# Performance work log

Measured on AMD Instinct MI355X. Metric: run time of the kernel, lower is better.

The kernel has to match this reference:

```python
import jax, jax.numpy as jnp
import numpy as np

EPS = 1e-5
N_NODES = 100000


def setup_inputs() -> dict:
    key = jax.random.key(0)
    ks = jax.random.split(key, 24)
    N, F = N_NODES, 64
    E = 1600000
    inp = {
        "x": jax.random.normal(ks[0], (N, F), dtype=jnp.float32),
        "edge_index": jax.random.randint(ks[1], (2, E), 0, N, dtype=jnp.int64),
    }
    dims = [(F, 32), (32, 64), (64, 128), (128, 1)]
    for i, (din, dout) in enumerate(dims, start=1):
        kw, kb = jax.random.split(ks[1 + i], 2)
        scale = 1.0 / np.sqrt(din)
        inp[f"W{i}"] = jax.random.uniform(kw, (din, dout), jnp.float32, -scale, scale)
        inp[f"b{i}"] = jax.random.uniform(kb, (dout,), jnp.float32, -scale, scale)
    for i, d in enumerate([32, 64, 128], start=1):
        kg, kbe, km, kv = jax.random.split(ks[8 + i], 4)
        inp[f"g{i}"] = 1.0 + 0.1 * jax.random.normal(kg, (d,), jnp.float32)
        inp[f"be{i}"] = 0.1 * jax.random.normal(kbe, (d,), jnp.float32)
        inp[f"rm{i}"] = 0.1 * jax.random.normal(km, (d,), jnp.float32)
        inp[f"rv{i}"] = 0.5 + jax.random.uniform(kv, (d,), jnp.float32)
    return inp


def _gcn_conv(x, src, dst, norm, W, b, n):
    # GCNConv: linear transform then D^-1/2 A_hat D^-1/2 aggregation (self-loops in src/dst)
    xw = x @ W  # [N, dout]
    msg = xw[src] * norm[:, None]  # [E+N, dout] gather
    return jax.ops.segment_sum(msg, dst, num_segments=n) + b


def _bn_eval(x, g, be, rm, rv):
    return (x - rm) * jax.lax.rsqrt(rv + EPS) * g + be


def reference(x, edge_index, W1, b1, W2, b2, W3, b3, W4, b4,
              g1, be1, rm1, rv1, g2, be2, rm2, rv2, g3, be3, rm3, rv3):
    n = x.shape[0]
    loop = jnp.arange(n, dtype=edge_index.dtype)
    src = jnp.concatenate([edge_index[0], loop])
    dst = jnp.concatenate([edge_index[1], loop])
    deg = jax.ops.segment_sum(jnp.ones_like(dst, dtype=x.dtype), dst, num_segments=n)
    dinv = jnp.where(deg > 0, jax.lax.rsqrt(deg), 0.0)
    norm = dinv[src] * dinv[dst]  # shared across layers

    h = _gcn_conv(x, src, dst, norm, W1, b1, n)
    h = jax.nn.elu(_bn_eval(h, g1, be1, rm1, rv1))
    h = _gcn_conv(h, src, dst, norm, W2, b2, n)
    h = jax.nn.elu(_bn_eval(h, g2, be2, rm2, rv2))
    h = _gcn_conv(h, src, dst, norm, W3, b3, n)
    h = jax.nn.elu(_bn_eval(h, g3, be3, rm3, rv3))
    h = _gcn_conv(h, src, dst, norm, W4, b4, n)
    return jax.nn.sigmoid(jax.nn.elu(h))
```

## Files before the change

kernel.cpp:

```cpp
#include <hip/hip_runtime.h>

#define EPSF 1e-5f
#define BKT_SHIFT 9
#define BKT_NODES 512
#define TILE_E 4096

__device__ __forceinline__ float elu_f(float x) { return x > 0.f ? x : expm1f(x); }


__global__ __launch_bounds__(256) void k_zero(int* p, int n) {
    int i = blockIdx.x * 256 + threadIdx.x;
    if (i < n) p[i] = 0;
}

__global__ __launch_bounds__(256) void k_bhist(const int* __restrict__ dst, int* __restrict__ bkt_cnt, int E) {
    __shared__ int h[256];
    int t = threadIdx.x;
    h[t] = 0;
    __syncthreads();
    for (long e = (long)blockIdx.x * 256 + t; e < E; e += (long)gridDim.x * 256)
        atomicAdd(&h[dst[e] >> BKT_SHIFT], 1);
    __syncthreads();
    if (h[t]) atomicAdd(&bkt_cnt[t], h[t]);
}

__global__ __launch_bounds__(256) void k_bscan(const int* __restrict__ bkt_cnt, int* __restrict__ bbase,
                                               int* __restrict__ cursor) {
    __shared__ int sh[256];
    int t = threadIdx.x;
    int v = bkt_cnt[t];
    sh[t] = v;
    __syncthreads();
    for (int off = 1; off < 256; off <<= 1) {
        int add = (t >= off) ? sh[t - off] : 0;
        __syncthreads();
        sh[t] += add;
        __syncthreads();
    }
    int ex = sh[t] - v;
    bbase[t] = ex;
    cursor[t] = ex;
}

__global__ __launch_bounds__(256) void k_bpart(const int* __restrict__ src, const int* __restrict__ dst,
                                               int* __restrict__ cursor, int2* __restrict__ csr_tmp, int E) {
    __shared__ int hcnt[256];
    __shared__ int gbase[256];
    int t = threadIdx.x;
    long tile0 = (long)blockIdx.x * TILE_E;
    hcnt[t] = 0;
    __syncthreads();
    int d[16], s[16], rk[16];
    #pragma unroll
    for (int j = 0; j < 16; ++j) {
        long e = tile0 + j * 256 + t;
        if (e < E) {
            d[j] = dst[e];
            s[j] = src[e];
            rk[j] = atomicAdd(&hcnt[d[j] >> BKT_SHIFT], 1);
        }
    }
    __syncthreads();
    int c = hcnt[t];
    if (c) gbase[t] = atomicAdd(&cursor[t], c);
    __syncthreads();
    #pragma unroll
    for (int j = 0; j < 16; ++j) {
        long e = tile0 + j * 256 + t;
        if (e < E) {
            int2 q;
            q.x = d[j];
            q.y = s[j];
            csr_tmp[gbase[d[j] >> BKT_SHIFT] + rk[j]] = q;
        }
    }
}

__global__ __launch_bounds__(256) void k_bfine(const int2* __restrict__ csr_tmp, const int* __restrict__ bbase,
                                               const int* __restrict__ bkt_cnt, int* __restrict__ cnt,
                                               int* __restrict__ base, float* __restrict__ dinv,
                                               int* __restrict__ csr_s, int N) {
    __shared__ int cnt5[BKT_NODES];
    __shared__ int off5[BKT_NODES];
    __shared__ int sh[256];
    int b = blockIdx.x;
    int t = threadIdx.x;
    int d0 = b << BKT_SHIFT;
    int bb = bbase[b];
    int bc = bkt_cnt[b];
    cnt5[t] = 0;
    cnt5[t + 256] = 0;
    __syncthreads();
    for (int k = t; k < bc; k += 256) atomicAdd(&cnt5[csr_tmp[bb + k].x - d0], 1);
    __syncthreads();
    int v0 = cnt5[2 * t], v1 = cnt5[2 * t + 1];
    int p = v0 + v1;
    sh[t] = p;
    __syncthreads();
    for (int off = 1; off < 256; off <<= 1) {
        int add = (t >= off) ? sh[t - off] : 0;
        __syncthreads();
        sh[t] += add;
        __syncthreads();
    }
    int pre = sh[t] - p;
    off5[2 * t] = pre;
    off5[2 * t + 1] = pre + v0;
    #pragma unroll
    for (int j = 0; j < 2; ++j) {
        int idx = 2 * t + j;
        int i = d0 + idx;
        if (i < N) {
            int c = cnt5[idx];
            base[i] = bb + off5[idx];
            cnt[i] = c;
            dinv[i] = rsqrtf((float)(c + 1));
        }
    }
    __syncthreads();
    for (int k = t; k < bc; k += 256) {
        int2 e = csr_tmp[bb + k];
        int pos = bb + atomicAdd(&off5[e.x - d0], 1);
        csr_s[pos] = e.y;
    }
}

__global__ __launch_bounds__(256) void k_csrw(const int* __restrict__ csr_s, const float* __restrict__ dinv,
                                              int2* __restrict__ csr_sw, int E) {
    for (long e = (long)blockIdx.x * 256 + threadIdx.x; e < E; e += (long)gridDim.x * 256) {
        int s = csr_s[e];
        int2 q;
        q.x = s;
        q.y = __float_as_int(dinv[s]);
        csr_sw[e] = q;
    }
}

template<int F, bool L1EPI>
__global__ __launch_bounds__(256) void k_gather(const int* __restrict__ base, const int* __restrict__ cnt,
                                                const int2* __restrict__ csr_sw,
                                                const float* __restrict__ dinv, const float* __restrict__ xin,
                                                const float* __restrict__ b, const float* __restrict__ g,
                                                const float* __restrict__ be, const float* __restrict__ rm,
                                                const float* __restrict__ rv, float* __restrict__ out, int n) {
    constexpr int C = F / 4;
    constexpr int NPB = 256 / C;
    int lane = threadIdx.x % C;
    int nl = threadIdx.x / C;
    int i = blockIdx.x * NPB + nl;
    if (i >= n) return;
    int k = base[i];
    int kend = k + cnt[i];
    float di = dinv[i];
    const float4* X4 = reinterpret_cast<const float4*>(xin);
    float4 acc = {0.f, 0.f, 0.f, 0.f};
    float4 acc2 = {0.f, 0.f, 0.f, 0.f};
    for (; k + 1 < kend; k += 2) {
        int2 ea = csr_sw[k];
        int2 eb = csr_sw[k + 1];
        float wa = __int_as_float(ea.y);
        float wb = __int_as_float(eb.y);
        float4 xa = X4[(long)ea.x * C + lane];
        float4 xb = X4[(long)eb.x * C + lane];
        acc.x += wa * xa.x; acc.y += wa * xa.y; acc.z += wa * xa.z; acc.w += wa * xa.w;
        acc2.x += wb * xb.x; acc2.y += wb * xb.y; acc2.z += wb * xb.z; acc2.w += wb * xb.w;
    }
    if (k < kend) {
        int2 ea = csr_sw[k];
        float wa = __int_as_float(ea.y);
        float4 xa = X4[(long)ea.x * C + lane];
        acc.x += wa * xa.x; acc.y += wa * xa.y; acc.z += wa * xa.z; acc.w += wa * xa.w;
    }
    acc.x += acc2.x; acc.y += acc2.y; acc.z += acc2.z; acc.w += acc2.w;
    float4 xs = X4[(long)i * C + lane];
    float4 o;
    o.x = di * (acc.x + di * xs.x);
    o.y = di * (acc.y + di * xs.y);
    o.z = di * (acc.z + di * xs.z);
    o.w = di * (acc.w + di * xs.w);
    if (L1EPI) {
        float4 bb = reinterpret_cast<const float4*>(b)[lane];
        float4 gg = reinterpret_cast<const float4*>(g)[lane];
        float4 ee = reinterpret_cast<const float4*>(be)[lane];
        float4 mm = reinterpret_cast<const float4*>(rm)[lane];
        float4 vv = reinterpret_cast<const float4*>(rv)[lane];
        o.x = elu_f((o.x + bb.x - mm.x) * rsqrtf(vv.x + EPSF) * gg.x + ee.x);
        o.y = elu_f((o.y + bb.y - mm.y) * rsqrtf(vv.y + EPSF) * gg.y + ee.y);
        o.z = elu_f((o.z + bb.z - mm.z) * rsqrtf(vv.z + EPSF) * gg.z + ee.z);
        o.w = elu_f((o.w + bb.w - mm.w) * rsqrtf(vv.w + EPSF) * gg.w + ee.w);
    }
    reinterpret_cast<float4*>(out)[(long)i * C + lane] = o;
}

__global__ __launch_bounds__(256) void k_gather1_final(const int* __restrict__ base, const int* __restrict__ cnt,
                                                       const int2* __restrict__ csr_sw,
                                                       const float* __restrict__ dinv, const float* __restrict__ y,
                                                       const float* __restrict__ b4, float* __restrict__ out, int n) {
    int i = blockIdx.x * 256 + threadIdx.x;
    if (i >= n) return;
    int k = base[i];
    int kend = k + cnt[i];
    float di = dinv[i];
    float acc = 0.f;
    for (; k < kend; ++k) {
        int2 ea = csr_sw[k];
        acc += __int_as_float(ea.y) * y[ea.x];
    }
    float v = di * (acc + di * y[i]) + b4[0];
    v = elu_f(v);
    out[i] = 1.f / (1.f + expf(-v));
}

template<int DIN, int DOUT, bool BN, bool FUSE_DOT>
__global__ __launch_bounds__(256, 4) void k_gemm_rt(const float* __restrict__ X, const float* __restrict__ W,
                                                    const float* __restrict__ b, const float* __restrict__ g,
                                                    const float* __restrict__ be, const float* __restrict__ rm,
                                                    const float* __restrict__ rv, const float* __restrict__ W4,
                                                    float* __restrict__ Y, int n) {
    constexpr int TR = 4;
    constexpr int FL = DOUT / 4;
    constexpr int RG = 256 / FL;
    constexpr int BR = RG * TR;
    __shared__ float Wl[DIN * DOUT];
    for (int idx = threadIdx.x; idx < DIN * DOUT; idx += 256) Wl[idx] = W[idx];
    __syncthreads();
    const int fl = threadIdx.x % FL;
    const int rg = threadIdx.x / FL;
    const int f0 = fl * 4;
    const long r0 = (long)blockIdx.x * BR + (long)rg * TR;

    float4 z; z.x = z.y = z.z = z.w = 0.f;
    float4 acc[TR];
    #pragma unroll
    for (int r = 0; r < TR; ++r) acc[r] = z;

    #pragma unroll 2
    for (int k0 = 0; k0 < DIN; k0 += 4) {
        float4 xv[TR];
        #pragma unroll
        for (int r = 0; r < TR; ++r) {
            long row = r0 + r;
            xv[r] = (row < n) ? *reinterpret_cast<const float4*>(X + row * DIN + k0) : z;
        }
        #pragma unroll
        for (int kk = 0; kk < 4; ++kk) {
            float4 w4 = *reinterpret_cast<const float4*>(&Wl[(k0 + kk) * DOUT + f0]);
            #pragma unroll
            for (int r = 0; r < TR; ++r) {
                float xs = (kk == 0) ? xv[r].x : (kk == 1) ? xv[r].y : (kk == 2) ? xv[r].z : xv[r].w;
                acc[r].x += xs * w4.x;
                acc[r].y += xs * w4.y;
                acc[r].z += xs * w4.z;
                acc[r].w += xs * w4.w;
            }
        }
    }

    float4 bias = z, scale = z, shift = z, w4d = z;
    if (BN) {
        bias = *reinterpret_cast<const float4*>(b + f0);
        float4 gg = *reinterpret_cast<const float4*>(g + f0);
        float4 ee = *reinterpret_cast<const float4*>(be + f0);
        float4 mm = *reinterpret_cast<const float4*>(rm + f0);
        float4 vv = *reinterpret_cast<const float4*>(rv + f0);
        scale.x = gg.x * rsqrtf(vv.x + EPSF); shift.x = ee.x - mm.x * scale.x;
        scale.y = gg.y * rsqrtf(vv.y + EPSF); shift.y = ee.y - mm.y * scale.y;
        scale.z = gg.z * rsqrtf(vv.z + EPSF); shift.z = ee.z - mm.z * scale.z;
        scale.w = gg.w * rsqrtf(vv.w + EPSF); shift.w = ee.w - mm.w * scale.w;
    }
    if (FUSE_DOT) w4d = *reinterpret_cast<const float4*>(W4 + f0);

    #pragma unroll
    for (int r = 0; r < TR; ++r) {
        long row = r0 + r;
        if (row >= n) continue;
        float4 v = acc[r];
        if (BN) {
            v.x = elu_f((v.x + bias.x) * scale.x + shift.x);
            v.y = elu_f((v.y + bias.y) * scale.y + shift.y);
            v.z = elu_f((v.z + bias.z) * scale.z + shift.z);
            v.w = elu_f((v.w + bias.w) * scale.w + shift.w);
        }
        if (FUSE_DOT) {
            float p = v.x * w4d.x + v.y * w4d.y + v.z * w4d.z + v.w * w4d.w;
            #pragma unroll
            for (int m = 1; m < FL; m <<= 1) p += __shfl_xor(p, m, 64);
            if (fl == 0) Y[row] = p;
        } else {
            *reinterpret_cast<float4*>(Y + row * DOUT + f0) = v;
        }
    }
}


extern "C" void kernel_launch(void* const* d_in, const int* in_sizes, int n_in,
                              void* d_out, int out_size, void* d_ws, size_t ws_size,
                              hipStream_t stream) {
    const float* x   = (const float*)d_in[0];
    const int*   edg = (const int*)d_in[1];
    const float* W1 = (const float*)d_in[2];
    const float* b1 = (const float*)d_in[3];
    const float* W2 = (const float*)d_in[4];
    const float* b2 = (const float*)d_in[5];
    const float* W3 = (const float*)d_in[6];
    const float* b3 = (const float*)d_in[7];
    const float* W4 = (const float*)d_in[8];
    const float* b4 = (const float*)d_in[9];
    const float* g1  = (const float*)d_in[10];
    const float* be1 = (const float*)d_in[11];
    const float* rm1 = (const float*)d_in[12];
    const float* rv1 = (const float*)d_in[13];
    const float* g2  = (const float*)d_in[14];
    const float* be2 = (const float*)d_in[15];
    const float* rm2 = (const float*)d_in[16];
    const float* rv2 = (const float*)d_in[17];
    const float* g3  = (const float*)d_in[18];
    const float* be3 = (const float*)d_in[19];
    const float* rm3 = (const float*)d_in[20];
    const float* rv3 = (const float*)d_in[21];
    float* out = (float*)d_out;

    const int N = in_sizes[0] / 64;
    const int E = in_sizes[1] / 2;
    const int* src = edg;
    const int* dst = edg + E;
    const int NB_BKT = (N + BKT_NODES - 1) / BKT_NODES;
    const int NTILES = (E + TILE_E - 1) / TILE_E;

    int*   bkt_cnt = (int*)d_ws;
    int*   bbase   = bkt_cnt + 256;
    int*   cursor  = bbase + 256;
    int*   cnt     = cursor + 256;
    int*   base    = cnt + N;
    float* dinv    = (float*)(base + N);
    int2*  csr_sw  = (int2*)(dinv + N);
    float* featA   = (float*)(csr_sw + E);
    float* featB   = featA + (size_t)N * 64;
    int2*  csr_tmp = (int2*)featA;
    int*   csr_s   = (int*)featB;

    auto nb = [](long total) { return (int)((total + 255) / 256); };

    k_zero<<<1, 256, 0, stream>>>(bkt_cnt, 256);
    k_bhist<<<512, 256, 0, stream>>>(dst, bkt_cnt, E);
    k_bscan<<<1, 256, 0, stream>>>(bkt_cnt, bbase, cursor);
    k_bpart<<<NTILES, 256, 0, stream>>>(src, dst, cursor, csr_tmp, E);
    k_bfine<<<NB_BKT, 256, 0, stream>>>(csr_tmp, bbase, bkt_cnt, cnt, base, dinv, csr_s, N);
    k_csrw<<<2048, 256, 0, stream>>>(csr_s, dinv, csr_sw, E);

    k_gemm_rt<64, 32, false, false><<<(N + 127) / 128, 256, 0, stream>>>(
        x, W1, nullptr, nullptr, nullptr, nullptr, nullptr, nullptr, featA, N);
    k_gather<32, true><<<(N + 31) / 32, 256, 0, stream>>>(base, cnt, csr_sw, dinv, featA,
                                                          b1, g1, be1, rm1, rv1, featB, N);

    k_gather<32, false><<<(N + 31) / 32, 256, 0, stream>>>(base, cnt, csr_sw, dinv, featB,
                                                           nullptr, nullptr, nullptr, nullptr, nullptr, featA, N);
    k_gemm_rt<32, 64, true, false><<<(N + 63) / 64, 256, 0, stream>>>(
        featA, W2, b2, g2, be2, rm2, rv2, nullptr, featB, N);

    k_gather<64, false><<<(N + 15) / 16, 256, 0, stream>>>(base, cnt, csr_sw, dinv, featB,
                                                           nullptr, nullptr, nullptr, nullptr, nullptr, featA, N);
    k_gemm_rt<64, 128, true, true><<<(N + 31) / 32, 256, 0, stream>>>(
        featA, W3, b3, g3, be3, rm3, rv3, W4, featB, N);

    k_gather1_final<<<nb(N), 256, 0, stream>>>(base, cnt, csr_sw, dinv, featB, b4, out, N);
}
```

Measured before the change: 422.4 us.

## Fold source-side normalization into producer epilogues and drop per-edge weights

Every node's features are now pre-scaled by its own dinv inside the producing kernel (GEMM epilogue or the layer-1 gather epilogue). Because of this, the aggregation only needs plain sums over neighbour indices. The CSR now stores bare 4-byte source indices instead of (index, weight) pairs, and the k_csrw pass that built the weighted CSR is removed. This cuts one edge-sized kernel and halves the index bytes streamed by every gather. The gather loop is also unrolled to four independent accumulators for more memory-level parallelism, and the workspace layout and ping-pong buffers are reassigned to match.

Result: faster. 399.0 us (-5.5%).

```diff
diff --git a/kernel.cpp b/kernel.cpp
--- a/kernel.cpp
+++ b/kernel.cpp
@@ -125,20 +125,9 @@
     }
 }
 
-__global__ __launch_bounds__(256) void k_csrw(const int* __restrict__ csr_s, const float* __restrict__ dinv,
-                                              int2* __restrict__ csr_sw, int E) {
-    for (long e = (long)blockIdx.x * 256 + threadIdx.x; e < E; e += (long)gridDim.x * 256) {
-        int s = csr_s[e];
-        int2 q;
-        q.x = s;
-        q.y = __float_as_int(dinv[s]);
-        csr_sw[e] = q;
-    }
-}
-
 template<int F, bool L1EPI>
 __global__ __launch_bounds__(256) void k_gather(const int* __restrict__ base, const int* __restrict__ cnt,
-                                                const int2* __restrict__ csr_sw,
+                                                const int* __restrict__ csr_s,
                                                 const float* __restrict__ dinv, const float* __restrict__ xin,
                                                 const float* __restrict__ b, const float* __restrict__ g,
                                                 const float* __restrict__ be, const float* __restrict__ rm,
@@ -153,47 +142,45 @@
     int kend = k + cnt[i];
     float di = dinv[i];
     const float4* X4 = reinterpret_cast<const float4*>(xin);
-    float4 acc = {0.f, 0.f, 0.f, 0.f};
-    float4 acc2 = {0.f, 0.f, 0.f, 0.f};
-    for (; k + 1 < kend; k += 2) {
-        int2 ea = csr_sw[k];
-        int2 eb = csr_sw[k + 1];
-        float wa = __int_as_float(ea.y);
-        float wb = __int_as_float(eb.y);
-        float4 xa = X4[(long)ea.x * C + lane];
-        float4 xb = X4[(long)eb.x * C + lane];
-        acc.x += wa * xa.x; acc.y += wa * xa.y; acc.z += wa * xa.z; acc.w += wa * xa.w;
-        acc2.x += wb * xb.x; acc2.y += wb * xb.y; acc2.z += wb * xb.z; acc2.w += wb * xb.w;
-    }
-    if (k < kend) {
-        int2 ea = csr_sw[k];
-        float wa = __int_as_float(ea.y);
-        float4 xa = X4[(long)ea.x * C + lane];
-        acc.x += wa * xa.x; acc.y += wa * xa.y; acc.z += wa * xa.z; acc.w += wa * xa.w;
-    }
-    acc.x += acc2.x; acc.y += acc2.y; acc.z += acc2.z; acc.w += acc2.w;
+    float4 z = {0.f, 0.f, 0.f, 0.f};
+    float4 a0 = z, a1 = z, a2 = z, a3 = z;
+    for (; k + 3 < kend; k += 4) {
+        int s0 = csr_s[k], s1 = csr_s[k + 1], s2 = csr_s[k + 2], s3 = csr_s[k + 3];
+        float4 x0 = X4[(long)s0 * C + lane];
+        float4 x1 = X4[(long)s1 * C + lane];
+        float4 x2 = X4[(long)s2 * C + lane];
+        float4 x3 = X4[(long)s3 * C + lane];
+        a0.x += x0.x; a0.y += x0.y; a0.z += x0.z; a0.w += x0.w;
+        a1.x += x1.x; a1.y += x1.y; a1.z += x1.z; a1.w += x1.w;
+        a2.x += x2.x; a2.y += x2.y; a2.z += x2.z; a2.w += x2.w;
+        a3.x += x3.x; a3.y += x3.y; a3.z += x3.z; a3.w += x3.w;
+    }
+    for (; k < kend; ++k) {
+        float4 xa = X4[(long)csr_s[k] * C + lane];
+        a0.x += xa.x; a0.y += xa.y; a0.z += xa.z; a0.w += xa.w;
+    }
     float4 xs = X4[(long)i * C + lane];
     float4 o;
-    o.x = di * (acc.x + di * xs.x);
-    o.y = di * (acc.y + di * xs.y);
-    o.z = di * (acc.z + di * xs.z);
-    o.w = di * (acc.w + di * xs.w);
+    o.x = di * (a0.x + a1.x + a2.x + a3.x + xs.x);
+    o.y = di * (a0.y + a1.y + a2.y + a3.y + xs.y);
+    o.z = di * (a0.z + a1.z + a2.z + a3.z + xs.z);
+    o.w = di * (a0.w + a1.w + a2.w + a3.w + xs.w);
     if (L1EPI) {
         float4 bb = reinterpret_cast<const float4*>(b)[lane];
         float4 gg = reinterpret_cast<const float4*>(g)[lane];
         float4 ee = reinterpret_cast<const float4*>(be)[lane];
         float4 mm = reinterpret_cast<const float4*>(rm)[lane];
         float4 vv = reinterpret_cast<const float4*>(rv)[lane];
-        o.x = elu_f((o.x + bb.x - mm.x) * rsqrtf(vv.x + EPSF) * gg.x + ee.x);
-        o.y = elu_f((o.y + bb.y - mm.y) * rsqrtf(vv.y + EPSF) * gg.y + ee.y);
-        o.z = elu_f((o.z + bb.z - mm.z) * rsqrtf(vv.z + EPSF) * gg.z + ee.z);
-        o.w = elu_f((o.w + bb.w - mm.w) * rsqrtf(vv.w + EPSF) * gg.w + ee.w);
+        o.x = di * elu_f((o.x + bb.x - mm.x) * rsqrtf(vv.x + EPSF) * gg.x + ee.x);
+        o.y = di * elu_f((o.y + bb.y - mm.y) * rsqrtf(vv.y + EPSF) * gg.y + ee.y);
+        o.z = di * elu_f((o.z + bb.z - mm.z) * rsqrtf(vv.z + EPSF) * gg.z + ee.z);
+        o.w = di * elu_f((o.w + bb.w - mm.w) * rsqrtf(vv.w + EPSF) * gg.w + ee.w);
     }
     reinterpret_cast<float4*>(out)[(long)i * C + lane] = o;
 }
 
 __global__ __launch_bounds__(256) void k_gather1_final(const int* __restrict__ base, const int* __restrict__ cnt,
-                                                       const int2* __restrict__ csr_sw,
+                                                       const int* __restrict__ csr_s,
                                                        const float* __restrict__ dinv, const float* __restrict__ y,
                                                        const float* __restrict__ b4, float* __restrict__ out, int n) {
     int i = blockIdx.x * 256 + threadIdx.x;
@@ -202,20 +189,18 @@
     int kend = k + cnt[i];
     float di = dinv[i];
     float acc = 0.f;
-    for (; k < kend; ++k) {
-        int2 ea = csr_sw[k];
-        acc += __int_as_float(ea.y) * y[ea.x];
-    }
-    float v = di * (acc + di * y[i]) + b4[0];
+    for (; k < kend; ++k) acc += y[csr_s[k]];
+    float v = di * (acc + y[i]) + b4[0];
     v = elu_f(v);
     out[i] = 1.f / (1.f + expf(-v));
 }
 
-template<int DIN, int DOUT, bool BN, bool FUSE_DOT>
+template<int DIN, int DOUT, bool BN, bool FUSE_DOT, bool SCALE_DINV>
 __global__ __launch_bounds__(256, 4) void k_gemm_rt(const float* __restrict__ X, const float* __restrict__ W,
                                                     const float* __restrict__ b, const float* __restrict__ g,
                                                     const float* __restrict__ be, const float* __restrict__ rm,
                                                     const float* __restrict__ rv, const float* __restrict__ W4,
+                                                    const float* __restrict__ dinv,
                                                     float* __restrict__ Y, int n) {
     constexpr int TR = 4;
     constexpr int FL = DOUT / 4;
@@ -281,12 +266,14 @@
             v.z = elu_f((v.z + bias.z) * scale.z + shift.z);
             v.w = elu_f((v.w + bias.w) * scale.w + shift.w);
         }
+        float dv = SCALE_DINV ? dinv[row] : 1.f;
         if (FUSE_DOT) {
             float p = v.x * w4d.x + v.y * w4d.y + v.z * w4d.z + v.w * w4d.w;
             #pragma unroll
             for (int m = 1; m < FL; m <<= 1) p += __shfl_xor(p, m, 64);
-            if (fl == 0) Y[row] = p;
+            if (fl == 0) Y[row] = dv * p;
         } else {
+            if (SCALE_DINV) { v.x *= dv; v.y *= dv; v.z *= dv; v.w *= dv; }
             *reinterpret_cast<float4*>(Y + row * DOUT + f0) = v;
         }
     }
@@ -333,11 +320,10 @@
     int*   cnt     = cursor + 256;
     int*   base    = cnt + N;
     float* dinv    = (float*)(base + N);
-    int2*  csr_sw  = (int2*)(dinv + N);
-    float* featA   = (float*)(csr_sw + E);
+    int*   csr_s   = (int*)(dinv + N);
+    float* featA   = (float*)(csr_s + E);
     float* featB   = featA + (size_t)N * 64;
     int2*  csr_tmp = (int2*)featA;
-    int*   csr_s   = (int*)featB;
 
     auto nb = [](long total) { return (int)((total + 255) / 256); };
 
@@ -346,22 +332,21 @@
     k_bscan<<<1, 256, 0, stream>>>(bkt_cnt, bbase, cursor);
     k_bpart<<<NTILES, 256, 0, stream>>>(src, dst, cursor, csr_tmp, E);
     k_bfine<<<NB_BKT, 256, 0, stream>>>(csr_tmp, bbase, bkt_cnt, cnt, base, dinv, csr_s, N);
-    k_csrw<<<2048, 256, 0, stream>>>(csr_s, dinv, csr_sw, E);
-
-    k_gemm_rt<64, 32, false, false><<<(N + 127) / 128, 256, 0, stream>>>(
-        x, W1, nullptr, nullptr, nullptr, nullptr, nullptr, nullptr, featA, N);
-    k_gather<32, true><<<(N + 31) / 32, 256, 0, stream>>>(base, cnt, csr_sw, dinv, featA,
-                                                          b1, g1, be1, rm1, rv1, featB, N);
-
-    k_gather<32, false><<<(N + 31) / 32, 256, 0, stream>>>(base, cnt, csr_sw, dinv, featB,
-                                                           nullptr, nullptr, nullptr, nullptr, nullptr, featA, N);
-    k_gemm_rt<32, 64, true, false><<<(N + 63) / 64, 256, 0, stream>>>(
-        featA, W2, b2, g2, be2, rm2, rv2, nullptr, featB, N);
-
-    k_gather<64, false><<<(N + 15) / 16, 256, 0, stream>>>(base, cnt, csr_sw, dinv, featB,
-                                                           nullptr, nullptr, nullptr, nullptr, nullptr, featA, N);
-    k_gemm_rt<64, 128, true, true><<<(N + 31) / 32, 256, 0, stream>>>(
-        featA, W3, b3, g3, be3, rm3, rv3, W4, featB, N);
-
-    k_gather1_final<<<nb(N), 256, 0, stream>>>(base, cnt, csr_sw, dinv, featB, b4, out, N);
-}
+
+    k_gemm_rt<64, 32, false, false, true><<<(N + 127) / 128, 256, 0, stream>>>(
+        x, W1, nullptr, nullptr, nullptr, nullptr, nullptr, nullptr, dinv, featB, N);
+    k_gather<32, true><<<(N + 31) / 32, 256, 0, stream>>>(base, cnt, csr_s, dinv, featB,
+                                                          b1, g1, be1, rm1, rv1, featA, N);
+
+    k_gather<32, false><<<(N + 31) / 32, 256, 0, stream>>>(base, cnt, csr_s, dinv, featA,
+                                                           nullptr, nullptr, nullptr, nullptr, nullptr, featB, N);
+    k_gemm_rt<32, 64, true, false, true><<<(N + 63) / 64, 256, 0, stream>>>(
+        featB, W2, b2, g2, be2, rm2, rv2, nullptr, dinv, featA, N);
+
+    k_gather<64, false><<<(N + 15) / 16, 256, 0, stream>>>(base, cnt, csr_s, dinv, featA,
+                                                           nullptr, nullptr, nullptr, nullptr, nullptr, featB, N);
+    k_gemm_rt<64, 128, true, true, true><<<(N + 31) / 32, 256, 0, stream>>>(
+        featB, W3, b3, g3, be3, rm3, rv3, W4, dinv, featA, N);
+
+    k_gather1_final<<<nb(N), 256, 0, stream>>>(base, cnt, csr_s, dinv, featA, b4, out, N);
+}
```
